# Kernel optimization log

Measured on AMD Instinct MI355X. Metric: run time of the kernel, lower is better.

The kernel has to match this reference:

```python
import jax, jax.numpy as jnp
import numpy as np
from math import ceil

SCALE = (0.25, 0.25)
IM_SIZE = (1080, 1920)
KERNEL_WIDTH = 4.0


def _cubic(x):
    absx = np.abs(x)
    absx2 = absx * absx
    absx3 = absx2 * absx
    return ((1.5 * absx3 - 2.5 * absx2 + 1) * (absx <= 1)
            + (-0.5 * absx3 + 2.5 * absx2 - 4 * absx + 2) * ((1 < absx) * (absx <= 2)))


def _contributions(in_length, out_length, scale):
    # MATLAB-style imresize contributions (matches the torch module's numpy code)
    if scale < 1:
        h = lambda v: scale * _cubic(scale * v)
        kernel_width = KERNEL_WIDTH / scale
    else:
        h = _cubic
        kernel_width = KERNEL_WIDTH
    x = np.arange(1, out_length + 1).astype(np.float64)
    u = x / scale + 0.5 * (1 - 1 / scale)
    left = np.floor(u - kernel_width / 2)
    P = int(ceil(kernel_width)) + 2
    ind = np.expand_dims(left, axis=1) + np.arange(P) - 1
    indices = ind.astype(np.int32)
    weights = h(np.expand_dims(u, axis=1) - indices - 1)
    weights = weights / np.sum(weights, axis=1, keepdims=True)
    aux = np.concatenate((np.arange(in_length), np.arange(in_length - 1, -1, -1))).astype(np.int32)
    indices = aux[np.mod(indices, aux.size)]
    keep = np.nonzero(np.any(weights, axis=0))[0]
    return weights[:, keep].astype(np.float32), indices[:, keep].astype(np.int64)


def setup_inputs() -> dict:
    key = jax.random.key(0)
    B, C = 8, 3
    H, W = IM_SIZE
    x = jax.random.normal(key, (B, C, H, W), dtype=jnp.float32)
    out_h = int(ceil(SCALE[0] * H))
    out_w = int(ceil(SCALE[1] * W))
    w_h, idx_h = _contributions(H, out_h, SCALE[0])
    w_w, idx_w = _contributions(W, out_w, SCALE[1])
    return {
        "x": x,
        "w_h": jnp.asarray(w_h), "idx_h": jnp.asarray(idx_h),
        "w_w": jnp.asarray(w_w), "idx_w": jnp.asarray(idx_w),
    }


def reference(x, w_h, idx_h, w_w, idx_w):
    # x: [B, C, H, W] -> work in [B, H, W, C] like the torch transpose dance
    xb = jnp.transpose(x, (0, 2, 3, 1))
    # scale is equal along both axes -> argsort order is [0, 1]: resize H then W
    # gather rows: [B, outH, P, W, C], contract over P with weights [outH, P]
    g = xb[:, idx_h, :, :]
    xb = jnp.einsum("op,bopwc->bowc", w_h, g)
    # gather cols: [B, outH, outW, P, C]
    g = xb[:, :, idx_w, :]
    xb = jnp.einsum("op,bhopc->bhoc", w_w, g)
    return jnp.transpose(xb, (0, 3, 1, 2))
```

## Files before the change

### kernel.cpp

```cpp
#include <hip/hip_runtime.h>

namespace {

constexpr int H  = 1080;
constexpr int W  = 1920;
constexpr int OH = 270;
constexpr int OW = 480;
constexpr int KT = 16;
constexpr int G  = 7;
constexpr int NCHUNK = 38;
constexpr int VSTRIDE = 1028;

constexpr int EDGE_FULL = 4 * OW;
constexpr int EDGE_TOT  = EDGE_FULL + (OH - 4) * 4;
constexpr int EDGE_YS   = 6;

__global__ __launch_bounds__(256) void bicubic_fused(
    const float* __restrict__ x,
    const float* __restrict__ wh,
    const int*   __restrict__ ih,
    const float* __restrict__ ww,
    const int*   __restrict__ iw,
    float*       __restrict__ out)
{
    __shared__ float vbuf[G * VSTRIDE];

    const int tid = threadIdx.x;
    const int bx  = blockIdx.x;
    const int by  = blockIdx.y;
    const int bc  = blockIdx.z;

    if (by >= NCHUNK) {
        const int e   = (by - NCHUNK) * 2 + bx;
        const int idx = e * 256 + tid;
        if (idx >= EDGE_TOT) return;

        int oh, ow;
        if (idx < EDGE_FULL) {
            int q = idx / OW;
            ow = idx - q * OW;
            oh = (q < 2) ? q : OH - 4 + q;
        } else {
            int t = idx - EDGE_FULL;
            int q = t & 3;
            oh = 2 + (t >> 2);
            ow = (q < 2) ? q : OW - 4 + q;
        }

        const float* __restrict__ img = x + (size_t)bc * ((size_t)H * W);

        float wt[KT];
        __builtin_memcpy(wt, ww + (size_t)ow * KT, sizeof(wt));
        int ir[KT];
        __builtin_memcpy(ir, iw + (size_t)ow * KT, sizeof(ir));

        bool fastc = true;
        #pragma unroll
        for (int k = 1; k < KT; ++k) fastc = fastc && (ir[k] == ir[0] + k);
        const int i0 = ir[0];

        float acc = 0.0f;
        #pragma unroll 4
        for (int kh = 0; kh < KT; ++kh) {
            const int   r = ih[oh * KT + kh];
            const float w = wh[oh * KT + kh];
            const float* row = img + (size_t)r * W;
            float h = 0.0f;
            if (fastc) {
                float v[KT];
                __builtin_memcpy(v, row + i0, sizeof(v));
                #pragma unroll
                for (int k = 0; k < KT; ++k) h = fmaf(v[k], wt[k], h);
            } else {
                #pragma unroll
                for (int k = 0; k < KT; ++k) h = fmaf(row[ir[k]], wt[k], h);
            }
            acc = fmaf(w, h, acc);
        }
        out[((size_t)bc * OH + oh) * OW + ow] = acc;
        return;
    }

    const int owb = bx ? 254 : 2;
    const int Nw  = bx ? 224 : 252;
    const int c0  = 4 * owb - 8;
    const int oh0 = 2 + G * by;
    const int r0  = 4 * oh0 - 6;

    float wr[KT];
    __builtin_memcpy(wr, wh + (size_t)oh0 * KT, sizeof(wr));

    int c = c0 + 4 * tid;
    if (c > W - 4) c = W - 4;
    const float* __restrict__ p =
        x + ((size_t)bc * H + (size_t)r0) * W + c;

    float acc[4][4];
    #pragma unroll
    for (int m = 0; m < 4; ++m)
        #pragma unroll
        for (int cc = 0; cc < 4; ++cc) acc[m][cc] = 0.0f;

    float cur[4][4];
    #pragma unroll
    for (int pp = 0; pp < 4; ++pp)
        __builtin_memcpy(cur[pp], p + (size_t)pp * W, 16);
    p += (size_t)4 * W;

    #pragma unroll 1
    for (int q = 0; q < G + 3; ++q) {
        float nxt[4][4];
        if (q < G + 2) {
            #pragma unroll
            for (int pp = 0; pp < 4; ++pp)
                __builtin_memcpy(nxt[pp], p + (size_t)pp * W, 16);
            p += (size_t)4 * W;
        }
        #pragma unroll
        for (int pp = 0; pp < 4; ++pp)
            #pragma unroll
            for (int cc = 0; cc < 4; ++cc) {
                const float v = cur[pp][cc];
                acc[0][cc] = fmaf(wr[pp],      v, acc[0][cc]);
                acc[1][cc] = fmaf(wr[4 + pp],  v, acc[1][cc]);
                acc[2][cc] = fmaf(wr[8 + pp],  v, acc[2][cc]);
                acc[3][cc] = fmaf(wr[12 + pp], v, acc[3][cc]);
            }
        if (q >= 3) {
            __builtin_memcpy(&vbuf[(q - 3) * VSTRIDE + 4 * tid + 2],
                             acc[3], 16);
        }
        #pragma unroll
        for (int cc = 0; cc < 4; ++cc) {
            acc[3][cc] = acc[2][cc];
            acc[2][cc] = acc[1][cc];
            acc[1][cc] = acc[0][cc];
            acc[0][cc] = 0.0f;
        }
        if (q < G + 2) {
            #pragma unroll
            for (int pp = 0; pp < 4; ++pp)
                #pragma unroll
                for (int cc = 0; cc < 4; ++cc) cur[pp][cc] = nxt[pp][cc];
        }
    }
    __syncthreads();

    if (tid < Nw) {
        const int ow = owb + tid;
        float wt[KT];
        __builtin_memcpy(wt, ww + (size_t)ow * KT, sizeof(wt));
        float* __restrict__ obase =
            out + ((size_t)bc * OH + oh0) * OW + ow;
        #pragma unroll
        for (int t = 0; t < G; ++t) {
            float v[KT];
            __builtin_memcpy(v, &vbuf[t * VSTRIDE + 4 * tid + 4], sizeof(v));
            float s0 = 0.f, s1 = 0.f;
            #pragma unroll
            for (int k = 0; k < KT; k += 2) {
                s0 = fmaf(v[k],     wt[k],     s0);
                s1 = fmaf(v[k + 1], wt[k + 1], s1);
            }
            obase[(size_t)t * OW] = s0 + s1;
        }
    }
}

__global__ __launch_bounds__(256) void bicubic_generic(
    const float* __restrict__ x,
    const float* __restrict__ wh,
    const int*   __restrict__ ih,
    const float* __restrict__ ww,
    const int*   __restrict__ iw,
    float*       __restrict__ out,
    int Kh, int Kw, int total)
{
    int t = blockIdx.x * blockDim.x + threadIdx.x;
    if (t >= total) return;
    int ow = t % OW;
    int oh = (t / OW) % OH;
    int bc = t / (OW * OH);
    const float* img = x + (size_t)bc * ((size_t)H * W);
    float acc = 0.0f;
    for (int kh = 0; kh < Kh; ++kh) {
        const int   r = ih[oh * Kh + kh];
        const float w = wh[oh * Kh + kh];
        const float* row = img + (size_t)r * W;
        float h = 0.0f;
        for (int k = 0; k < Kw; ++k)
            h = fmaf(row[iw[ow * Kw + k]], ww[ow * Kw + k], h);
        acc = fmaf(w, h, acc);
    }
    out[t] = acc;
}

}

extern "C" void kernel_launch(void* const* d_in, const int* in_sizes, int n_in,
                              void* d_out, int out_size, void* d_ws, size_t ws_size,
                              hipStream_t stream) {
    const float* x  = (const float*)d_in[0];
    const float* wh = (const float*)d_in[1];
    const int*   ih = (const int*)d_in[2];
    const float* ww = (const float*)d_in[3];
    const int*   iw = (const int*)d_in[4];
    float*       out = (float*)d_out;

    const int BC = in_sizes[0] / (H * W);
    const int Kh = in_sizes[1] / OH;
    const int Kw = in_sizes[3] / OW;

    if (Kh == KT && Kw == KT) {
        dim3 grid(2, NCHUNK + EDGE_YS, BC);
        bicubic_fused<<<grid, 256, 0, stream>>>(x, wh, ih, ww, iw, out);
    } else {
        int total = BC * OH * OW;
        bicubic_generic<<<(total + 255) / 256, 256, 0, stream>>>(
            x, wh, ih, ww, iw, out, Kh, Kw, total);
    }
}
```

Measured before the change: 337.7 us.

## Shrink row-chunk to two output rows per block and fully unroll vertical pass

Reduces output rows per block from 7 to 2, which raises the block count and drops the rolling 4-stage accumulator pipeline. Each thread now loads 20 rows directly with a fully unrolled loop into two accumulators. Edge blocks move to the front of the grid, and the edge path's vertical loop is fully unrolled. This trades more redundant input row reads (halo overlap of 12 rows per 8 new rows) for more parallelism and simpler code with lower latency.

```diff
diff --git a/kernel.cpp b/kernel.cpp
--- a/kernel.cpp
+++ b/kernel.cpp
@@ -7,9 +7,10 @@
 constexpr int OH = 270;
 constexpr int OW = 480;
 constexpr int KT = 16;
-constexpr int G  = 7;
-constexpr int NCHUNK = 38;
-constexpr int VSTRIDE = 1028;
+constexpr int G  = 2;
+constexpr int NCHUNK = 133;
+constexpr int ROWS = 4 * G + 12;
+constexpr int VSTRIDE = 1032;
 
 constexpr int EDGE_FULL = 4 * OW;
 constexpr int EDGE_TOT  = EDGE_FULL + (OH - 4) * 4;
@@ -30,9 +31,8 @@
     const int by  = blockIdx.y;
     const int bc  = blockIdx.z;
 
-    if (by >= NCHUNK) {
-        const int e   = (by - NCHUNK) * 2 + bx;
-        const int idx = e * 256 + tid;
+    if (by < EDGE_YS) {
+        const int idx = (by * 2 + bx) * 256 + tid;
         if (idx >= EDGE_TOT) return;
 
         int oh, ow;
@@ -60,7 +60,7 @@
         const int i0 = ir[0];
 
         float acc = 0.0f;
-        #pragma unroll 4
+        #pragma unroll
         for (int kh = 0; kh < KT; ++kh) {
             const int   r = ih[oh * KT + kh];
             const float w = wh[oh * KT + kh];
@@ -84,7 +84,7 @@
     const int owb = bx ? 254 : 2;
     const int Nw  = bx ? 224 : 252;
     const int c0  = 4 * owb - 8;
-    const int oh0 = 2 + G * by;
+    const int oh0 = 2 + G * (by - EDGE_YS);
     const int r0  = 4 * oh0 - 6;
 
     float wr[KT];
@@ -95,55 +95,25 @@
     const float* __restrict__ p =
         x + ((size_t)bc * H + (size_t)r0) * W + c;
 
-    float acc[4][4];
+    float a0[4] = {0.f, 0.f, 0.f, 0.f};
+    float a1[4] = {0.f, 0.f, 0.f, 0.f};
     #pragma unroll
-    for (int m = 0; m < 4; ++m)
-        #pragma unroll
-        for (int cc = 0; cc < 4; ++cc) acc[m][cc] = 0.0f;
-
-    float cur[4][4];
-    #pragma unroll
-    for (int pp = 0; pp < 4; ++pp)
-        __builtin_memcpy(cur[pp], p + (size_t)pp * W, 16);
-    p += (size_t)4 * W;
-
-    #pragma unroll 1
-    for (int q = 0; q < G + 3; ++q) {
-        float nxt[4][4];
-        if (q < G + 2) {
+    for (int r = 0; r < ROWS; ++r) {
+        float v[4];
+        __builtin_memcpy(v, p + (size_t)r * W, 16);
+        if (r < 16) {
+            const float w = wr[r];
             #pragma unroll
-            for (int pp = 0; pp < 4; ++pp)
-                __builtin_memcpy(nxt[pp], p + (size_t)pp * W, 16);
-            p += (size_t)4 * W;
+            for (int cc = 0; cc < 4; ++cc) a0[cc] = fmaf(w, v[cc], a0[cc]);
         }
-        #pragma unroll
-        for (int pp = 0; pp < 4; ++pp)
+        if (r >= 4) {
+            const float w = wr[r - 4];
             #pragma unroll
-            for (int cc = 0; cc < 4; ++cc) {
-                const float v = cur[pp][cc];
-                acc[0][cc] = fmaf(wr[pp],      v, acc[0][cc]);
-                acc[1][cc] = fmaf(wr[4 + pp],  v, acc[1][cc]);
-                acc[2][cc] = fmaf(wr[8 + pp],  v, acc[2][cc]);
-                acc[3][cc] = fmaf(wr[12 + pp], v, acc[3][cc]);
-            }
-        if (q >= 3) {
-            __builtin_memcpy(&vbuf[(q - 3) * VSTRIDE + 4 * tid + 2],
-                             acc[3], 16);
-        }
-        #pragma unroll
-        for (int cc = 0; cc < 4; ++cc) {
-            acc[3][cc] = acc[2][cc];
-            acc[2][cc] = acc[1][cc];
-            acc[1][cc] = acc[0][cc];
-            acc[0][cc] = 0.0f;
-        }
-        if (q < G + 2) {
-            #pragma unroll
-            for (int pp = 0; pp < 4; ++pp)
-                #pragma unroll
-                for (int cc = 0; cc < 4; ++cc) cur[pp][cc] = nxt[pp][cc];
+            for (int cc = 0; cc < 4; ++cc) a1[cc] = fmaf(w, v[cc], a1[cc]);
         }
     }
+    __builtin_memcpy(&vbuf[0 * VSTRIDE + 4 * tid + 2], a0, 16);
+    __builtin_memcpy(&vbuf[1 * VSTRIDE + 4 * tid + 2], a1, 16);
     __syncthreads();
 
     if (tid < Nw) {
@@ -212,7 +182,7 @@
     const int Kw = in_sizes[3] / OW;
 
     if (Kh == KT && Kw == KT) {
-        dim3 grid(2, NCHUNK + EDGE_YS, BC);
+        dim3 grid(2, EDGE_YS + NCHUNK, BC);
         bicubic_fused<<<grid, 256, 0, stream>>>(x, wh, ih, ww, iw, out);
     } else {
         int total = BC * OH * OW;
```

New measurement: 321.4 us. -4.8%, faster.
